# Optimization experiments

Hardware: AMD Instinct MI355X
Metric: run time of the kernel (lower is better)

Reference implementation:

```python
import jax, jax.numpy as jnp
import numpy as np

SIZE_DICT = 512
DIM_DICT = 64
TEMPERATURE = 0.5
EPS = 1e-10


def setup_inputs() -> dict:
    key = jax.random.key(0)
    k1, k2, k3 = jax.random.split(key, 3)
    bs, dz, W, H = 32, 64, 32, 32
    z = jax.random.normal(k1, (bs, dz, W, H), dtype=jnp.float32)
    var_q = jnp.ones((1,), dtype=jnp.float32)
    codebook = jax.random.normal(k2, (SIZE_DICT, DIM_DICT), dtype=jnp.float32)
    gumbel_u = jax.random.uniform(k3, (bs * W * H, SIZE_DICT), dtype=jnp.float32)
    return {"z_from_encoder": z, "var_q": var_q, "codebook": codebook, "gumbel_u": gumbel_u}


def reference(z_from_encoder, var_q, codebook, gumbel_u):
    bs, dz, W, H = z_from_encoder.shape
    # permute to channels-last and flatten: [N, D]
    z_flat = jnp.transpose(z_from_encoder, (0, 2, 3, 1)).reshape(-1, dz)
    # precision with clamping as in torch code
    precision_q = jnp.clip(1.0 / jnp.clip(var_q, 1e-5, None), None, 1e5)  # [1]
    half_prec = 0.5 * precision_q
    # squared euclidean distances to codebook: [N, K]
    dist = (jnp.sum(z_flat ** 2, axis=1, keepdims=True)
            + jnp.sum(codebook ** 2, axis=1)
            - 2.0 * z_flat @ codebook.T)
    logit = -half_prec * dist
    logit = logit - jnp.max(logit, axis=-1, keepdims=True)
    logit = jnp.clip(logit, -50.0, 50.0)
    probabilities = jax.nn.softmax(logit, axis=-1)
    log_probabilities = jax.nn.log_softmax(logit, axis=-1)
    # Gumbel-softmax sampling (training path)
    g = -jnp.log(-jnp.log(gumbel_u + EPS) + EPS)
    encodings = jax.nn.softmax((logit + g) / TEMPERATURE, axis=-1)
    # soft codebook lookup
    z_quantized = (encodings @ codebook).reshape(bs, W, H, dz)
    z_to_decoder = jnp.transpose(z_quantized, (0, 3, 1, 2))  # [bs, D, W, H]
    # discrete KLD term: sum_{n,k} p log p / bs
    kld_discrete = jnp.sum(probabilities * log_probabilities) / bs
    # continuous KLD term: mean over batch of weighted squared error
    kld_continuous = jnp.mean(
        jnp.sum((z_from_encoder - z_to_decoder) ** 2 * half_prec, axis=(1, 2, 3)))
    loss = kld_discrete + kld_continuous
    # perplexity from detached probabilities
    avg_probs = jnp.clip(jnp.mean(jax.lax.stop_gradient(probabilities), axis=0), 1e-10, None)
    perplexity = jnp.exp(-jnp.sum(avg_probs * jnp.log(avg_probs + 1e-10)))
    return z_to_decoder, loss, perplexity
```

## Files before the change

kernel.cpp:

```cpp
#include <hip/hip_runtime.h>


typedef _Float16 half8 __attribute__((ext_vector_type(8)));
typedef float f32x4 __attribute__((ext_vector_type(4)));

#define WS_B1   4096
#define WS_B2   20480
#define WS_PROB 36864
#define WS_LOSS 299008
#define WS_RED  303104
#define WS_NEED 319488

#define SMEM_PRE 24064
#define SMEM_FB  155136

#define LOG2E 1.4426950408889634f
#define LN2   0.6931471805599453f
#define C2G   1.4426950408889634e-10f

__device__ __forceinline__ float half_prec(const float* var_q) {
  float vq = var_q[0];
  float pq = fminf(1.0f / fmaxf(vq, 1e-5f), 1e5f);
  return 0.5f * pq;
}

__global__ void k_pre(const float* __restrict__ var_q,
                      const float* __restrict__ cb,
                      float* __restrict__ ws, int pre) {
  int t = threadIdx.x, wg = blockIdx.x;
  if (wg == 0) {
    float hp = half_prec(var_q);
    if (t == 0) ws[512] = 0.0f;
    ws[516 + t] = 0.0f;
    const float4* row = (const float4*)(cb + t * 64);
    float s = 0.0f;
    #pragma unroll
    for (int i = 0; i < 16; ++i) {
      float4 v = row[i];
      s += v.x*v.x + v.y*v.y + v.z*v.z + v.w*v.w;
    }
    ws[t] = hp * s * LOG2E;
  }
  if (!pre) return;
  int gid = wg * 512 + t;
  if (gid < 4096) {
    int l = gid & 63, grp = gid >> 6;
    int tt = grp >> 1, kk = grp & 1;
    int cc = l & 15, gg = l >> 4;
    const float* src = cb + (cc*32 + tt)*64 + kk*32 + gg*8;
    float4 v0 = *(const float4*)src;
    float4 v1 = *(const float4*)(src + 4);
    half8 h = { (_Float16)v0.x, (_Float16)v0.y, (_Float16)v0.z, (_Float16)v0.w,
                (_Float16)v1.x, (_Float16)v1.y, (_Float16)v1.z, (_Float16)v1.w };
    ((half8*)(ws + WS_B1))[gid] = h;
  } else {
    int F = gid - 4096;
    int l = F & 63, grp = F >> 6;
    int kt = grp >> 2, nt = grp & 3;
    int cc = l & 15, gg = l >> 4;
    int dim = nt*16 + cc;
    half8 h;
    #pragma unroll
    for (int j = 0; j < 8; ++j) {
      int kap = gg*8 + j;
      int code = ((kap & 15) << 5) + 2*kt + (kap >> 4);
      h[j] = (_Float16)cb[code*64 + dim];
    }
    ((half8*)(ws + WS_B2))[F] = h;
  }
}

template <int PRE>
__global__ __launch_bounds__(512) void k_main_t(
    const float* __restrict__ z, const float* __restrict__ vq,
    const float* __restrict__ cb, const float* __restrict__ gu,
    float* __restrict__ out, float* __restrict__ ws)
{
  extern __shared__ char smem[];
  constexpr int CB = PRE ? 0 : 131072;
  char*  chunkAll = smem + CB;
  float* pr   = (float*)(smem + CB + 20480);
  float* redM = (float*)(smem + CB + 22528);
  float* redS = (float*)(smem + CB + 23040);
  float* redP = (float*)(smem + CB + 23552);

  const int tid  = threadIdx.x;
  const int lane = tid & 63;
  const int wv   = tid >> 6;
  const int h    = wv & 1;
  const int p    = wv >> 1;
  const int c    = lane & 15;
  const int g    = lane >> 4;

  pr[tid] = 0.0f;

  const half8* B1;
  const half8* B2;
  if constexpr (PRE) {
    B1 = (const half8*)(ws + WS_B1);
    B2 = (const half8*)(ws + WS_B2);
  } else {
    _Float16* lB1 = (_Float16*)smem;
    _Float16* lB2 = (_Float16*)(smem + 65536);
    #pragma unroll
    for (int i = 0; i < 8; ++i) {
      int F = tid + 512*i;
      int l = F & 63, grp = F >> 6;
      int t = grp >> 1, kk = grp & 1;
      int cc = l & 15, gg = l >> 4;
      const float* src = cb + (cc*32 + t)*64 + kk*32 + gg*8;
      float4 v0 = *(const float4*)src;
      float4 v1 = *(const float4*)(src + 4);
      half8 hh = { (_Float16)v0.x, (_Float16)v0.y, (_Float16)v0.z, (_Float16)v0.w,
                   (_Float16)v1.x, (_Float16)v1.y, (_Float16)v1.z, (_Float16)v1.w };
      ((half8*)lB1)[F] = hh;
    }
    #pragma unroll
    for (int i = 0; i < 8; ++i) {
      int F = tid + 512*i;
      int l = F & 63, grp = F >> 6;
      int kt = grp >> 2, nt = grp & 3;
      int cc = l & 15, gg = l >> 4;
      int dim = nt*16 + cc;
      half8 hh;
      #pragma unroll
      for (int j = 0; j < 8; ++j) {
        int kap = gg*8 + j;
        int code = ((kap & 15) << 5) + 2*kt + (kap >> 4);
        hh[j] = (_Float16)cb[code*64 + dim];
      }
      ((half8*)lB2)[F] = hh;
    }
    B1 = (const half8*)lB1;
    B2 = (const half8*)lB2;
  }

  const float hp   = half_prec(vq);
  const float s2hp = 2.0f * hp * LOG2E;

  const int row0 = (blockIdx.x * 4 + p) * 16;
  const int b    = row0 >> 10;
  const int wh0  = row0 & 1023;

  _Float16* zc = (_Float16*)(chunkAll + p * 5120);

  float zr[8];
  {
    const float* zp = z + ((size_t)(b*64 + lane) << 10) + wh0 + 8*h;
    float4 v0 = *(const float4*)zp;
    float4 v1 = *(const float4*)(zp + 4);
    zr[0]=v0.x; zr[1]=v0.y; zr[2]=v0.z; zr[3]=v0.w;
    zr[4]=v1.x; zr[5]=v1.y; zr[6]=v1.z; zr[7]=v1.w;
  }
  #pragma unroll
  for (int s = 0; s < 8; ++s) zc[(8*h + s)*72 + lane] = (_Float16)(zr[s] * s2hp);

  __syncthreads();

  f32x4 acc[16];
  {
    const float4* hn = (const float4*)(ws + c*32 + h*16);
    #pragma unroll
    for (int u = 0; u < 4; ++u) {
      float4 h4 = hn[u];
      acc[4*u+0] = (f32x4){-h4.x, -h4.x, -h4.x, -h4.x};
      acc[4*u+1] = (f32x4){-h4.y, -h4.y, -h4.y, -h4.y};
      acc[4*u+2] = (f32x4){-h4.z, -h4.z, -h4.z, -h4.z};
      acc[4*u+3] = (f32x4){-h4.w, -h4.w, -h4.w, -h4.w};
    }
  }

  half8 zA0 = *(const half8*)(zc + c*72 + g*8);
  half8 zA1 = *(const half8*)(zc + c*72 + 32 + g*8);

  #pragma unroll
  for (int t = 0; t < 16; ++t) {
    int tt = h*16 + t;
    acc[t] = __builtin_amdgcn_mfma_f32_16x16x32_f16(zA0, B1[(tt*2+0)*64 + lane], acc[t], 0, 0, 0);
    acc[t] = __builtin_amdgcn_mfma_f32_16x16x32_f16(zA1, B1[(tt*2+1)*64 + lane], acc[t], 0, 0, 0);
  }

  const float* gub = gu + ((size_t)(row0 + 4*g))*512 + c*32 + h*16;
  float4 ubA[4], ubB[4];
  #pragma unroll
  for (int tt = 0; tt < 4; ++tt) ubA[tt] = *(const float4*)(gub + tt*4);

  const int rix = p*32 + h*16;

  #pragma unroll
  for (int q = 0; q < 4; ++q) {
    float m = acc[0][q];
    #pragma unroll
    for (int t = 1; t < 16; ++t) m = fmaxf(m, acc[t][q]);
    #pragma unroll
    for (int o = 8; o > 0; o >>= 1) m = fmaxf(m, __shfl_xor(m, o));
    if (c == 0) redM[rix + 4*g + q] = m;
  }
  __syncthreads();
  float mq[4];
  #pragma unroll
  for (int q = 0; q < 4; ++q)
    mq[q] = fmaxf(redM[p*32 + 4*g + q], redM[p*32 + 16 + 4*g + q]);

  {
    float s1[4] = {0,0,0,0}, pl[4] = {0,0,0,0};
    #pragma unroll
    for (int t = 0; t < 16; ++t)
      #pragma unroll
      for (int q = 0; q < 4; ++q) {
        float l = acc[t][q] - mq[q];
        float e = exp2f(l);
        s1[q] += e;
        pl[q] = fmaf(e, l, pl[q]);
        acc[t][q] = e;
      }
    #pragma unroll
    for (int q = 0; q < 4; ++q) {
      #pragma unroll
      for (int o = 8; o > 0; o >>= 1) { s1[q] += __shfl_xor(s1[q], o); pl[q] += __shfl_xor(pl[q], o); }
      if (c == 0) { redS[rix + 4*g + q] = s1[q]; redP[rix + 4*g + q] = pl[q]; }
    }
  }
  __syncthreads();
  float kd = 0.0f, inv1[4];
  #pragma unroll
  for (int q = 0; q < 4; ++q) {
    float S = redS[p*32 + 4*g + q] + redS[p*32 + 16 + 4*g + q];
    float P = redP[p*32 + 4*g + q] + redP[p*32 + 16 + 4*g + q];
    inv1[q] = 1.0f / S;
    kd += P * inv1[q] - __log2f(S);
  }

  #pragma unroll
  for (int t = 0; t < 16; ++t) {
    float v = 0.0f;
    #pragma unroll
    for (int q = 0; q < 4; ++q) v = fmaf(acc[t][q], inv1[q], v);
    v += __shfl_xor(v, 16);
    v += __shfl_xor(v, 32);
    if (g == 0) atomicAdd(&pr[(h*16 + t)*16 + c], v);
  }

  #pragma unroll
  for (int q = 0; q < 4; ++q) {
    const float4* cur = (q & 1) ? ubB : ubA;
    float4*       nxt = (q & 1) ? ubA : ubB;
    if (q < 3) {
      #pragma unroll
      for (int tt = 0; tt < 4; ++tt) nxt[tt] = *(const float4*)(gub + (q+1)*512 + tt*4);
    }
    #pragma unroll
    for (int tt = 0; tt < 4; ++tt) {
      float4 u4 = cur[tt];
      float y0 = C2G - __log2f(u4.x + 1e-10f);
      float y1 = C2G - __log2f(u4.y + 1e-10f);
      float y2 = C2G - __log2f(u4.z + 1e-10f);
      float y3 = C2G - __log2f(u4.w + 1e-10f);
      float t0 = acc[4*tt+0][q] * __builtin_amdgcn_rcpf(y0);
      float t1 = acc[4*tt+1][q] * __builtin_amdgcn_rcpf(y1);
      float t2 = acc[4*tt+2][q] * __builtin_amdgcn_rcpf(y2);
      float t3 = acc[4*tt+3][q] * __builtin_amdgcn_rcpf(y3);
      acc[4*tt+0][q] = t0*t0;
      acc[4*tt+1][q] = t1*t1;
      acc[4*tt+2][q] = t2*t2;
      acc[4*tt+3][q] = t3*t3;
    }
  }

  __syncthreads();

  #pragma unroll
  for (int q = 0; q < 4; ++q) {
    float s = 0.0f;
    #pragma unroll
    for (int t = 0; t < 16; ++t) s += acc[t][q];
    #pragma unroll
    for (int o = 8; o > 0; o >>= 1) s += __shfl_xor(s, o);
    if (c == 0) redS[rix + 4*g + q] = s;
  }
  __syncthreads();
  #pragma unroll
  for (int q = 0; q < 4; ++q) {
    float inv = 1.0f / (redS[p*32 + 4*g + q] + redS[p*32 + 16 + 4*g + q]);
    #pragma unroll
    for (int t = 0; t < 16; ++t) acc[t][q] *= inv;
  }

  f32x4 zacc[4];
  #pragma unroll
  for (int nt = 0; nt < 4; ++nt) zacc[nt] = (f32x4){0.f, 0.f, 0.f, 0.f};

  _Float16* myES = (_Float16*)(chunkAll + wv * 2560);
  #pragma unroll
  for (int k = 0; k < 8; ++k) {
    _Float16* eS = myES + (k & 1) * 640;
    #pragma unroll
    for (int tb = 0; tb < 2; ++tb)
      #pragma unroll
      for (int q = 0; q < 4; ++q)
        eS[(4*g + q)*40 + 16*tb + c] = (_Float16)acc[2*k + tb][q];
    half8 ea = *(const half8*)(eS + c*40 + g*8);
    int kt = h*8 + k;
    #pragma unroll
    for (int nt = 0; nt < 4; ++nt)
      zacc[nt] = __builtin_amdgcn_mfma_f32_16x16x32_f16(ea, B2[(kt*4 + nt)*64 + lane], zacc[nt], 0, 0, 0);
  }

  __syncthreads();
  float* zqx = (float*)chunkAll + p * 1056;
  if (h) {
    #pragma unroll
    for (int nt = 0; nt < 4; ++nt)
      #pragma unroll
      for (int q = 0; q < 4; ++q)
        zqx[(4*g + q)*66 + nt*16 + c] = zacc[nt][q];
  }
  __syncthreads();
  if (!h) {
    #pragma unroll
    for (int nt = 0; nt < 4; ++nt)
      #pragma unroll
      for (int q = 0; q < 4; ++q) {
        int ix = (4*g + q)*66 + nt*16 + c;
        zqx[ix] += zacc[nt][q];
      }
  }
  __syncthreads();

  float kc = 0.0f;
  {
    float* orow = out + ((size_t)(b*64 + lane) << 10) + wh0 + 8*h;
    float4 o0, o1;
    o0.x = zqx[(8*h + 0)*66 + lane]; o0.y = zqx[(8*h + 1)*66 + lane];
    o0.z = zqx[(8*h + 2)*66 + lane]; o0.w = zqx[(8*h + 3)*66 + lane];
    o1.x = zqx[(8*h + 4)*66 + lane]; o1.y = zqx[(8*h + 5)*66 + lane];
    o1.z = zqx[(8*h + 6)*66 + lane]; o1.w = zqx[(8*h + 7)*66 + lane];
    float d;
    d = zr[0]-o0.x; kc = fmaf(d,d,kc);  d = zr[1]-o0.y; kc = fmaf(d,d,kc);
    d = zr[2]-o0.z; kc = fmaf(d,d,kc);  d = zr[3]-o0.w; kc = fmaf(d,d,kc);
    d = zr[4]-o1.x; kc = fmaf(d,d,kc);  d = zr[5]-o1.y; kc = fmaf(d,d,kc);
    d = zr[6]-o1.z; kc = fmaf(d,d,kc);  d = zr[7]-o1.w; kc = fmaf(d,d,kc);
    *(float4*)orow       = o0;
    *(float4*)(orow + 4) = o1;
  }
  kc *= hp;

  float lv = (h ? 0.0f : kd * (0.0625f * LN2)) + kc;
  #pragma unroll
  for (int o = 32; o > 0; o >>= 1) lv += __shfl_xor(lv, o);
  if (lane == 0) {
    if constexpr (PRE) ws[WS_LOSS + blockIdx.x*8 + wv] = lv;
    else               atomicAdd(&ws[512], lv);
  }

  __syncthreads();
  if constexpr (PRE) {
    ws[WS_PROB + (size_t)blockIdx.x*512 + tid] = pr[tid];
  } else {
    atomicAdd(ws + 516 + tid, pr[tid]);
  }
}

__global__ void k_red(float* __restrict__ ws) {
  int gix = blockIdx.x, t = threadIdx.x;
  float s = 0.0f;
  #pragma unroll 4
  for (int i = 0; i < 16; ++i) s += ws[WS_PROB + (size_t)(gix*16 + i)*512 + t];
  ws[WS_RED + gix*512 + t] = s;
}

__global__ void k_fin(const float* __restrict__ ws, float* __restrict__ out, int pre) {
  __shared__ float redH[16], redL[16];
  int t = threadIdx.x;
  float h = 0.0f, l = 0.0f;
  if (pre) {
    if (t < 512) {
      float s = 0.0f;
      #pragma unroll
      for (int g = 0; g < 32; ++g) s += ws[WS_RED + g*512 + t];
      float a = fmaxf(s * (1.0f/32768.0f), 1e-10f);
      h = -a * __logf(a + 1e-10f);
    } else {
      int x = t - 512;
      #pragma unroll
      for (int i = 0; i < 8; ++i) l += ws[WS_LOSS + x + 512*i];
    }
  } else {
    if (t < 512) {
      float a = fmaxf(ws[516 + t] * (1.0f/32768.0f), 1e-10f);
      h = -a * __logf(a + 1e-10f);
    } else if (t == 512) {
      l = ws[512];
    }
  }
  #pragma unroll
  for (int o = 32; o > 0; o >>= 1) { h += __shfl_xor(h, o); l += __shfl_xor(l, o); }
  if ((t & 63) == 0) { redH[t >> 6] = h; redL[t >> 6] = l; }
  __syncthreads();
  if (t == 0) {
    float H = 0.0f, L = 0.0f;
    #pragma unroll
    for (int i = 0; i < 16; ++i) { H += redH[i]; L += redL[i]; }
    out[2097152] = L * (1.0f/32.0f);
    out[2097153] = __expf(H);
  }
}

extern "C" void kernel_launch(void* const* d_in, const int* in_sizes, int n_in,
                              void* d_out, int out_size, void* d_ws, size_t ws_size,
                              hipStream_t stream) {
  const float* z  = (const float*)d_in[0];
  const float* vq = (const float*)d_in[1];
  const float* cb = (const float*)d_in[2];
  const float* gu = (const float*)d_in[3];
  float* out = (float*)d_out;
  float* ws  = (float*)d_ws;
  int pre = (ws_size >= (size_t)WS_NEED * 4) ? 1 : 0;

  hipLaunchKernelGGL(k_pre, dim3(16), dim3(512), 0, stream, vq, cb, ws, pre);
  if (pre) {
    hipLaunchKernelGGL(k_main_t<1>, dim3(512), dim3(512), SMEM_PRE, stream, z, vq, cb, gu, out, ws);
    hipLaunchKernelGGL(k_red, dim3(32), dim3(512), 0, stream, ws);
  } else {
    hipFuncSetAttribute((const void*)&k_main_t<0>, hipFuncAttributeMaxDynamicSharedMemorySize, SMEM_FB);
    hipLaunchKernelGGL(k_main_t<0>, dim3(512), dim3(512), SMEM_FB, stream, z, vq, cb, gu, out, ws);
  }
  hipLaunchKernelGGL(k_fin, dim3(1), dim3(1024), 0, stream, ws, out, pre);
}
```

Before: 65.42 us.

## Split each row chunk across four waves with 1024-thread blocks

The precomputed-codebook path now uses 1024-thread blocks, so four waves share each 16-row chunk instead of two. Each wave handles 128 codes, which halves the accumulator registers per wave and raises the wave count. Cross-wave max, sum and z-quantized reductions are extended to four partials, with an extra shared-memory staging buffer. The gumbel prefetch double-buffering is dropped in favour of direct loads. The fallback path is split out into its own non-templated kernel.

```diff
diff --git a/kernel.cpp b/kernel.cpp
--- a/kernel.cpp
+++ b/kernel.cpp
@@ -11,7 +11,15 @@
 #define WS_RED  303104
 #define WS_NEED 319488
 
-#define SMEM_PRE 24064
+#define ZC_OFF  0
+#define ES_OFF  9216
+#define ZQ_OFF  50176
+#define PR_OFF  83968
+#define RM_OFF  86016
+#define RS_OFF  87040
+#define RP_OFF  88064
+#define LB_OFF  89088
+#define SMEM_PRE 89152
 #define SMEM_FB  155136
 
 #define LOG2E 1.4426950408889634f
@@ -70,70 +78,30 @@
   }
 }
 
-template <int PRE>
-__global__ __launch_bounds__(512) void k_main_t(
+__global__ __launch_bounds__(1024) void k_main_pre(
     const float* __restrict__ z, const float* __restrict__ vq,
     const float* __restrict__ cb, const float* __restrict__ gu,
     float* __restrict__ out, float* __restrict__ ws)
 {
   extern __shared__ char smem[];
-  constexpr int CB = PRE ? 0 : 131072;
-  char*  chunkAll = smem + CB;
-  float* pr   = (float*)(smem + CB + 20480);
-  float* redM = (float*)(smem + CB + 22528);
-  float* redS = (float*)(smem + CB + 23040);
-  float* redP = (float*)(smem + CB + 23552);
+  float* pr   = (float*)(smem + PR_OFF);
+  float* redM = (float*)(smem + RM_OFF);
+  float* redS = (float*)(smem + RS_OFF);
+  float* redP = (float*)(smem + RP_OFF);
+  float* lb   = (float*)(smem + LB_OFF);
 
   const int tid  = threadIdx.x;
   const int lane = tid & 63;
   const int wv   = tid >> 6;
-  const int h    = wv & 1;
-  const int p    = wv >> 1;
+  const int e    = wv & 3;
+  const int p    = wv >> 2;
   const int c    = lane & 15;
   const int g    = lane >> 4;
 
-  pr[tid] = 0.0f;
-
-  const half8* B1;
-  const half8* B2;
-  if constexpr (PRE) {
-    B1 = (const half8*)(ws + WS_B1);
-    B2 = (const half8*)(ws + WS_B2);
-  } else {
-    _Float16* lB1 = (_Float16*)smem;
-    _Float16* lB2 = (_Float16*)(smem + 65536);
-    #pragma unroll
-    for (int i = 0; i < 8; ++i) {
-      int F = tid + 512*i;
-      int l = F & 63, grp = F >> 6;
-      int t = grp >> 1, kk = grp & 1;
-      int cc = l & 15, gg = l >> 4;
-      const float* src = cb + (cc*32 + t)*64 + kk*32 + gg*8;
-      float4 v0 = *(const float4*)src;
-      float4 v1 = *(const float4*)(src + 4);
-      half8 hh = { (_Float16)v0.x, (_Float16)v0.y, (_Float16)v0.z, (_Float16)v0.w,
-                   (_Float16)v1.x, (_Float16)v1.y, (_Float16)v1.z, (_Float16)v1.w };
-      ((half8*)lB1)[F] = hh;
-    }
-    #pragma unroll
-    for (int i = 0; i < 8; ++i) {
-      int F = tid + 512*i;
-      int l = F & 63, grp = F >> 6;
-      int kt = grp >> 2, nt = grp & 3;
-      int cc = l & 15, gg = l >> 4;
-      int dim = nt*16 + cc;
-      half8 hh;
-      #pragma unroll
-      for (int j = 0; j < 8; ++j) {
-        int kap = gg*8 + j;
-        int code = ((kap & 15) << 5) + 2*kt + (kap >> 4);
-        hh[j] = (_Float16)cb[code*64 + dim];
-      }
-      ((half8*)lB2)[F] = hh;
-    }
-    B1 = (const half8*)lB1;
-    B2 = (const half8*)lB2;
-  }
+  if (tid < 512) pr[tid] = 0.0f;
+
+  const half8* B1 = (const half8*)(ws + WS_B1);
+  const half8* B2 = (const half8*)(ws + WS_B2);
 
   const float hp   = half_prec(vq);
   const float s2hp = 2.0f * hp * LOG2E;
@@ -142,26 +110,24 @@
   const int b    = row0 >> 10;
   const int wh0  = row0 & 1023;
 
-  _Float16* zc = (_Float16*)(chunkAll + p * 5120);
-
-  float zr[8];
-  {
-    const float* zp = z + ((size_t)(b*64 + lane) << 10) + wh0 + 8*h;
+  _Float16* zc = (_Float16*)(smem + ZC_OFF + p * 2304);
+
+  float zr[4];
+  {
+    const float* zp = z + ((size_t)(b*64 + lane) << 10) + wh0 + 4*e;
     float4 v0 = *(const float4*)zp;
-    float4 v1 = *(const float4*)(zp + 4);
     zr[0]=v0.x; zr[1]=v0.y; zr[2]=v0.z; zr[3]=v0.w;
-    zr[4]=v1.x; zr[5]=v1.y; zr[6]=v1.z; zr[7]=v1.w;
-  }
-  #pragma unroll
-  for (int s = 0; s < 8; ++s) zc[(8*h + s)*72 + lane] = (_Float16)(zr[s] * s2hp);
-
-  __syncthreads();
-
-  f32x4 acc[16];
-  {
-    const float4* hn = (const float4*)(ws + c*32 + h*16);
-    #pragma unroll
-    for (int u = 0; u < 4; ++u) {
+  }
+  #pragma unroll
+  for (int s = 0; s < 4; ++s) zc[(4*e + s)*72 + lane] = (_Float16)(zr[s] * s2hp);
+
+  __syncthreads();
+
+  f32x4 acc[8];
+  {
+    const float4* hn = (const float4*)(ws + c*32 + 8*e);
+    #pragma unroll
+    for (int u = 0; u < 2; ++u) {
       float4 h4 = hn[u];
       acc[4*u+0] = (f32x4){-h4.x, -h4.x, -h4.x, -h4.x};
       acc[4*u+1] = (f32x4){-h4.y, -h4.y, -h4.y, -h4.y};
@@ -174,24 +140,19 @@
   half8 zA1 = *(const half8*)(zc + c*72 + 32 + g*8);
 
   #pragma unroll
-  for (int t = 0; t < 16; ++t) {
-    int tt = h*16 + t;
+  for (int t = 0; t < 8; ++t) {
+    int tt = 8*e + t;
     acc[t] = __builtin_amdgcn_mfma_f32_16x16x32_f16(zA0, B1[(tt*2+0)*64 + lane], acc[t], 0, 0, 0);
     acc[t] = __builtin_amdgcn_mfma_f32_16x16x32_f16(zA1, B1[(tt*2+1)*64 + lane], acc[t], 0, 0, 0);
   }
 
-  const float* gub = gu + ((size_t)(row0 + 4*g))*512 + c*32 + h*16;
-  float4 ubA[4], ubB[4];
-  #pragma unroll
-  for (int tt = 0; tt < 4; ++tt) ubA[tt] = *(const float4*)(gub + tt*4);
-
-  const int rix = p*32 + h*16;
+  const int rix = p*64 + e*16;
 
   #pragma unroll
   for (int q = 0; q < 4; ++q) {
     float m = acc[0][q];
     #pragma unroll
-    for (int t = 1; t < 16; ++t) m = fmaxf(m, acc[t][q]);
+    for (int t = 1; t < 8; ++t) m = fmaxf(m, acc[t][q]);
     #pragma unroll
     for (int o = 8; o > 0; o >>= 1) m = fmaxf(m, __shfl_xor(m, o));
     if (c == 0) redM[rix + 4*g + q] = m;
@@ -199,20 +160,22 @@
   __syncthreads();
   float mq[4];
   #pragma unroll
-  for (int q = 0; q < 4; ++q)
-    mq[q] = fmaxf(redM[p*32 + 4*g + q], redM[p*32 + 16 + 4*g + q]);
+  for (int q = 0; q < 4; ++q) {
+    int ix = p*64 + 4*g + q;
+    mq[q] = fmaxf(fmaxf(redM[ix], redM[ix+16]), fmaxf(redM[ix+32], redM[ix+48]));
+  }
 
   {
     float s1[4] = {0,0,0,0}, pl[4] = {0,0,0,0};
     #pragma unroll
-    for (int t = 0; t < 16; ++t)
+    for (int t = 0; t < 8; ++t)
       #pragma unroll
       for (int q = 0; q < 4; ++q) {
         float l = acc[t][q] - mq[q];
-        float e = exp2f(l);
-        s1[q] += e;
-        pl[q] = fmaf(e, l, pl[q]);
-        acc[t][q] = e;
+        float ev = exp2f(l);
+        s1[q] += ev;
+        pl[q] = fmaf(ev, l, pl[q]);
+        acc[t][q] = ev;
       }
     #pragma unroll
     for (int q = 0; q < 4; ++q) {
@@ -225,33 +188,29 @@
   float kd = 0.0f, inv1[4];
   #pragma unroll
   for (int q = 0; q < 4; ++q) {
-    float S = redS[p*32 + 4*g + q] + redS[p*32 + 16 + 4*g + q];
-    float P = redP[p*32 + 4*g + q] + redP[p*32 + 16 + 4*g + q];
+    int ix = p*64 + 4*g + q;
+    float S = (redS[ix] + redS[ix+16]) + (redS[ix+32] + redS[ix+48]);
+    float P = (redP[ix] + redP[ix+16]) + (redP[ix+32] + redP[ix+48]);
     inv1[q] = 1.0f / S;
     kd += P * inv1[q] - __log2f(S);
   }
 
   #pragma unroll
-  for (int t = 0; t < 16; ++t) {
+  for (int t = 0; t < 8; ++t) {
     float v = 0.0f;
     #pragma unroll
     for (int q = 0; q < 4; ++q) v = fmaf(acc[t][q], inv1[q], v);
     v += __shfl_xor(v, 16);
     v += __shfl_xor(v, 32);
-    if (g == 0) atomicAdd(&pr[(h*16 + t)*16 + c], v);
-  }
-
-  #pragma unroll
-  for (int q = 0; q < 4; ++q) {
-    const float4* cur = (q & 1) ? ubB : ubA;
-    float4*       nxt = (q & 1) ? ubA : ubB;
-    if (q < 3) {
-      #pragma unroll
-      for (int tt = 0; tt < 4; ++tt) nxt[tt] = *(const float4*)(gub + (q+1)*512 + tt*4);
-    }
-    #pragma unroll
-    for (int tt = 0; tt < 4; ++tt) {
-      float4 u4 = cur[tt];
+    if (g == 0) atomicAdd(&pr[(8*e + t)*16 + c], v);
+  }
+
+  #pragma unroll
+  for (int q = 0; q < 4; ++q) {
+    const float4* ub = (const float4*)(gu + ((size_t)(row0 + 4*g + q))*512 + c*32 + 8*e);
+    #pragma unroll
+    for (int tt = 0; tt < 2; ++tt) {
+      float4 u4 = ub[tt];
       float y0 = C2G - __log2f(u4.x + 1e-10f);
       float y1 = C2G - __log2f(u4.y + 1e-10f);
       float y2 = C2G - __log2f(u4.z + 1e-10f);
@@ -273,6 +232,272 @@
   for (int q = 0; q < 4; ++q) {
     float s = 0.0f;
     #pragma unroll
+    for (int t = 0; t < 8; ++t) s += acc[t][q];
+    #pragma unroll
+    for (int o = 8; o > 0; o >>= 1) s += __shfl_xor(s, o);
+    if (c == 0) redS[rix + 4*g + q] = s;
+  }
+  __syncthreads();
+  #pragma unroll
+  for (int q = 0; q < 4; ++q) {
+    int ix = p*64 + 4*g + q;
+    float inv = 1.0f / ((redS[ix] + redS[ix+16]) + (redS[ix+32] + redS[ix+48]));
+    #pragma unroll
+    for (int t = 0; t < 8; ++t) acc[t][q] *= inv;
+  }
+
+  f32x4 zacc[4];
+  #pragma unroll
+  for (int nt = 0; nt < 4; ++nt) zacc[nt] = (f32x4){0.f, 0.f, 0.f, 0.f};
+
+  _Float16* myES = (_Float16*)(smem + ES_OFF + wv * 2560);
+  #pragma unroll
+  for (int k = 0; k < 4; ++k) {
+    _Float16* eS = myES + (k & 1) * 640;
+    #pragma unroll
+    for (int tb = 0; tb < 2; ++tb)
+      #pragma unroll
+      for (int q = 0; q < 4; ++q)
+        eS[(4*g + q)*40 + 16*tb + c] = (_Float16)acc[2*k + tb][q];
+    half8 ea = *(const half8*)(eS + c*40 + g*8);
+    int kt = 4*e + k;
+    #pragma unroll
+    for (int nt = 0; nt < 4; ++nt)
+      zacc[nt] = __builtin_amdgcn_mfma_f32_16x16x32_f16(ea, B2[(kt*4 + nt)*64 + lane], zacc[nt], 0, 0, 0);
+  }
+
+  float* zqA = (float*)(smem + ZQ_OFF + p * 8448);
+  float* zqB = zqA + 1056;
+  if (e & 1) {
+    float* zqX = (e == 1) ? zqA : zqB;
+    #pragma unroll
+    for (int nt = 0; nt < 4; ++nt)
+      #pragma unroll
+      for (int q = 0; q < 4; ++q)
+        zqX[(4*g + q)*66 + nt*16 + c] = zacc[nt][q];
+  }
+  __syncthreads();
+  if (!(e & 1)) {
+    float* zqX = (e == 0) ? zqA : zqB;
+    #pragma unroll
+    for (int nt = 0; nt < 4; ++nt)
+      #pragma unroll
+      for (int q = 0; q < 4; ++q)
+        zqX[(4*g + q)*66 + nt*16 + c] += zacc[nt][q];
+  }
+  __syncthreads();
+
+  float kc = 0.0f;
+  {
+    float* orow = out + ((size_t)(b*64 + lane) << 10) + wh0 + 4*e;
+    float4 ov;
+    ov.x = zqA[(4*e + 0)*66 + lane] + zqB[(4*e + 0)*66 + lane];
+    ov.y = zqA[(4*e + 1)*66 + lane] + zqB[(4*e + 1)*66 + lane];
+    ov.z = zqA[(4*e + 2)*66 + lane] + zqB[(4*e + 2)*66 + lane];
+    ov.w = zqA[(4*e + 3)*66 + lane] + zqB[(4*e + 3)*66 + lane];
+    float d;
+    d = zr[0]-ov.x; kc = fmaf(d,d,kc);  d = zr[1]-ov.y; kc = fmaf(d,d,kc);
+    d = zr[2]-ov.z; kc = fmaf(d,d,kc);  d = zr[3]-ov.w; kc = fmaf(d,d,kc);
+    *(float4*)orow = ov;
+  }
+  kc *= hp;
+
+  float lv = ((e == 0) ? kd * (0.0625f * LN2) : 0.0f) + kc;
+  #pragma unroll
+  for (int o = 32; o > 0; o >>= 1) lv += __shfl_xor(lv, o);
+  if (lane == 0) lb[p*4 + e] = lv;
+  __syncthreads();
+  if (e == 0 && lane == 0)
+    ws[WS_LOSS + blockIdx.x*4 + p] = (lb[p*4+0] + lb[p*4+1]) + (lb[p*4+2] + lb[p*4+3]);
+
+  if (tid < 512) ws[WS_PROB + (size_t)blockIdx.x*512 + tid] = pr[tid];
+}
+
+__global__ __launch_bounds__(512) void k_main_fb(
+    const float* __restrict__ z, const float* __restrict__ vq,
+    const float* __restrict__ cb, const float* __restrict__ gu,
+    float* __restrict__ out, float* __restrict__ ws)
+{
+  extern __shared__ char smem[];
+  constexpr int CB = 131072;
+  char*  chunkAll = smem + CB;
+  float* pr   = (float*)(smem + CB + 20480);
+  float* redM = (float*)(smem + CB + 22528);
+  float* redS = (float*)(smem + CB + 23040);
+  float* redP = (float*)(smem + CB + 23552);
+
+  const int tid  = threadIdx.x;
+  const int lane = tid & 63;
+  const int wv   = tid >> 6;
+  const int h    = wv & 1;
+  const int p    = wv >> 1;
+  const int c    = lane & 15;
+  const int g    = lane >> 4;
+
+  pr[tid] = 0.0f;
+
+  _Float16* lB1 = (_Float16*)smem;
+  _Float16* lB2 = (_Float16*)(smem + 65536);
+  #pragma unroll
+  for (int i = 0; i < 8; ++i) {
+    int F = tid + 512*i;
+    int l = F & 63, grp = F >> 6;
+    int t = grp >> 1, kk = grp & 1;
+    int cc = l & 15, gg = l >> 4;
+    const float* src = cb + (cc*32 + t)*64 + kk*32 + gg*8;
+    float4 v0 = *(const float4*)src;
+    float4 v1 = *(const float4*)(src + 4);
+    half8 hh = { (_Float16)v0.x, (_Float16)v0.y, (_Float16)v0.z, (_Float16)v0.w,
+                 (_Float16)v1.x, (_Float16)v1.y, (_Float16)v1.z, (_Float16)v1.w };
+    ((half8*)lB1)[F] = hh;
+  }
+  #pragma unroll
+  for (int i = 0; i < 8; ++i) {
+    int F = tid + 512*i;
+    int l = F & 63, grp = F >> 6;
+    int kt = grp >> 2, nt = grp & 3;
+    int cc = l & 15, gg = l >> 4;
+    int dim = nt*16 + cc;
+    half8 hh;
+    #pragma unroll
+    for (int j = 0; j < 8; ++j) {
+      int kap = gg*8 + j;
+      int code = ((kap & 15) << 5) + 2*kt + (kap >> 4);
+      hh[j] = (_Float16)cb[code*64 + dim];
+    }
+    ((half8*)lB2)[F] = hh;
+  }
+  const half8* B1 = (const half8*)lB1;
+  const half8* B2 = (const half8*)lB2;
+
+  const float hp   = half_prec(vq);
+  const float s2hp = 2.0f * hp * LOG2E;
+
+  const int row0 = (blockIdx.x * 4 + p) * 16;
+  const int b    = row0 >> 10;
+  const int wh0  = row0 & 1023;
+
+  _Float16* zc = (_Float16*)(chunkAll + p * 5120);
+
+  float zr[8];
+  {
+    const float* zp = z + ((size_t)(b*64 + lane) << 10) + wh0 + 8*h;
+    float4 v0 = *(const float4*)zp;
+    float4 v1 = *(const float4*)(zp + 4);
+    zr[0]=v0.x; zr[1]=v0.y; zr[2]=v0.z; zr[3]=v0.w;
+    zr[4]=v1.x; zr[5]=v1.y; zr[6]=v1.z; zr[7]=v1.w;
+  }
+  #pragma unroll
+  for (int s = 0; s < 8; ++s) zc[(8*h + s)*72 + lane] = (_Float16)(zr[s] * s2hp);
+
+  __syncthreads();
+
+  f32x4 acc[16];
+  {
+    const float4* hn = (const float4*)(ws + c*32 + h*16);
+    #pragma unroll
+    for (int u = 0; u < 4; ++u) {
+      float4 h4 = hn[u];
+      acc[4*u+0] = (f32x4){-h4.x, -h4.x, -h4.x, -h4.x};
+      acc[4*u+1] = (f32x4){-h4.y, -h4.y, -h4.y, -h4.y};
+      acc[4*u+2] = (f32x4){-h4.z, -h4.z, -h4.z, -h4.z};
+      acc[4*u+3] = (f32x4){-h4.w, -h4.w, -h4.w, -h4.w};
+    }
+  }
+
+  half8 zA0 = *(const half8*)(zc + c*72 + g*8);
+  half8 zA1 = *(const half8*)(zc + c*72 + 32 + g*8);
+
+  #pragma unroll
+  for (int t = 0; t < 16; ++t) {
+    int tt = h*16 + t;
+    acc[t] = __builtin_amdgcn_mfma_f32_16x16x32_f16(zA0, B1[(tt*2+0)*64 + lane], acc[t], 0, 0, 0);
+    acc[t] = __builtin_amdgcn_mfma_f32_16x16x32_f16(zA1, B1[(tt*2+1)*64 + lane], acc[t], 0, 0, 0);
+  }
+
+  const int rix = p*32 + h*16;
+
+  #pragma unroll
+  for (int q = 0; q < 4; ++q) {
+    float m = acc[0][q];
+    #pragma unroll
+    for (int t = 1; t < 16; ++t) m = fmaxf(m, acc[t][q]);
+    #pragma unroll
+    for (int o = 8; o > 0; o >>= 1) m = fmaxf(m, __shfl_xor(m, o));
+    if (c == 0) redM[rix + 4*g + q] = m;
+  }
+  __syncthreads();
+  float mq[4];
+  #pragma unroll
+  for (int q = 0; q < 4; ++q)
+    mq[q] = fmaxf(redM[p*32 + 4*g + q], redM[p*32 + 16 + 4*g + q]);
+
+  {
+    float s1[4] = {0,0,0,0}, pl[4] = {0,0,0,0};
+    #pragma unroll
+    for (int t = 0; t < 16; ++t)
+      #pragma unroll
+      for (int q = 0; q < 4; ++q) {
+        float l = acc[t][q] - mq[q];
+        float ev = exp2f(l);
+        s1[q] += ev;
+        pl[q] = fmaf(ev, l, pl[q]);
+        acc[t][q] = ev;
+      }
+    #pragma unroll
+    for (int q = 0; q < 4; ++q) {
+      #pragma unroll
+      for (int o = 8; o > 0; o >>= 1) { s1[q] += __shfl_xor(s1[q], o); pl[q] += __shfl_xor(pl[q], o); }
+      if (c == 0) { redS[rix + 4*g + q] = s1[q]; redP[rix + 4*g + q] = pl[q]; }
+    }
+  }
+  __syncthreads();
+  float kd = 0.0f, inv1[4];
+  #pragma unroll
+  for (int q = 0; q < 4; ++q) {
+    float S = redS[p*32 + 4*g + q] + redS[p*32 + 16 + 4*g + q];
+    float P = redP[p*32 + 4*g + q] + redP[p*32 + 16 + 4*g + q];
+    inv1[q] = 1.0f / S;
+    kd += P * inv1[q] - __log2f(S);
+  }
+
+  #pragma unroll
+  for (int t = 0; t < 16; ++t) {
+    float v = 0.0f;
+    #pragma unroll
+    for (int q = 0; q < 4; ++q) v = fmaf(acc[t][q], inv1[q], v);
+    v += __shfl_xor(v, 16);
+    v += __shfl_xor(v, 32);
+    if (g == 0) atomicAdd(&pr[(h*16 + t)*16 + c], v);
+  }
+
+  #pragma unroll
+  for (int q = 0; q < 4; ++q) {
+    const float4* ub = (const float4*)(gu + ((size_t)(row0 + 4*g + q))*512 + c*32 + h*16);
+    #pragma unroll
+    for (int tt = 0; tt < 4; ++tt) {
+      float4 u4 = ub[tt];
+      float y0 = C2G - __log2f(u4.x + 1e-10f);
+      float y1 = C2G - __log2f(u4.y + 1e-10f);
+      float y2 = C2G - __log2f(u4.z + 1e-10f);
+      float y3 = C2G - __log2f(u4.w + 1e-10f);
+      float t0 = acc[4*tt+0][q] * __builtin_amdgcn_rcpf(y0);
+      float t1 = acc[4*tt+1][q] * __builtin_amdgcn_rcpf(y1);
+      float t2 = acc[4*tt+2][q] * __builtin_amdgcn_rcpf(y2);
+      float t3 = acc[4*tt+3][q] * __builtin_amdgcn_rcpf(y3);
+      acc[4*tt+0][q] = t0*t0;
+      acc[4*tt+1][q] = t1*t1;
+      acc[4*tt+2][q] = t2*t2;
+      acc[4*tt+3][q] = t3*t3;
+    }
+  }
+
+  __syncthreads();
+
+  #pragma unroll
+  for (int q = 0; q < 4; ++q) {
+    float s = 0.0f;
+    #pragma unroll
     for (int t = 0; t < 16; ++t) s += acc[t][q];
     #pragma unroll
     for (int o = 8; o > 0; o >>= 1) s += __shfl_xor(s, o);
@@ -320,10 +545,8 @@
     #pragma unroll
     for (int nt = 0; nt < 4; ++nt)
       #pragma unroll
-      for (int q = 0; q < 4; ++q) {
-        int ix = (4*g + q)*66 + nt*16 + c;
-        zqx[ix] += zacc[nt][q];
-      }
+      for (int q = 0; q < 4; ++q)
+        zqx[(4*g + q)*66 + nt*16 + c] += zacc[nt][q];
   }
   __syncthreads();
 
@@ -348,17 +571,10 @@
   float lv = (h ? 0.0f : kd * (0.0625f * LN2)) + kc;
   #pragma unroll
   for (int o = 32; o > 0; o >>= 1) lv += __shfl_xor(lv, o);
-  if (lane == 0) {
-    if constexpr (PRE) ws[WS_LOSS + blockIdx.x*8 + wv] = lv;
-    else               atomicAdd(&ws[512], lv);
-  }
-
-  __syncthreads();
-  if constexpr (PRE) {
-    ws[WS_PROB + (size_t)blockIdx.x*512 + tid] = pr[tid];
-  } else {
-    atomicAdd(ws + 516 + tid, pr[tid]);
-  }
+  if (lane == 0) atomicAdd(&ws[512], lv);
+
+  __syncthreads();
+  atomicAdd(ws + 516 + tid, pr[tid]);
 }
 
 __global__ void k_red(float* __restrict__ ws) {
@@ -383,7 +599,7 @@
     } else {
       int x = t - 512;
       #pragma unroll
-      for (int i = 0; i < 8; ++i) l += ws[WS_LOSS + x + 512*i];
+      for (int i = 0; i < 4; ++i) l += ws[WS_LOSS + x + 512*i];
     }
   } else {
     if (t < 512) {
@@ -419,11 +635,12 @@
 
   hipLaunchKernelGGL(k_pre, dim3(16), dim3(512), 0, stream, vq, cb, ws, pre);
   if (pre) {
-    hipLaunchKernelGGL(k_main_t<1>, dim3(512), dim3(512), SMEM_PRE, stream, z, vq, cb, gu, out, ws);
+    hipFuncSetAttribute((const void*)k_main_pre, hipFuncAttributeMaxDynamicSharedMemorySize, SMEM_PRE);
+    hipLaunchKernelGGL(k_main_pre, dim3(512), dim3(1024), SMEM_PRE, stream, z, vq, cb, gu, out, ws);
     hipLaunchKernelGGL(k_red, dim3(32), dim3(512), 0, stream, ws);
   } else {
-    hipFuncSetAttribute((const void*)&k_main_t<0>, hipFuncAttributeMaxDynamicSharedMemorySize, SMEM_FB);
-    hipLaunchKernelGGL(k_main_t<0>, dim3(512), dim3(512), SMEM_FB, stream, z, vq, cb, gu, out, ws);
+    hipFuncSetAttribute((const void*)k_main_fb, hipFuncAttributeMaxDynamicSharedMemorySize, SMEM_FB);
+    hipLaunchKernelGGL(k_main_fb, dim3(512), dim3(512), SMEM_FB, stream, z, vq, cb, gu, out, ws);
   }
   hipLaunchKernelGGL(k_fin, dim3(1), dim3(1024), 0, stream, ws, out, pre);
 }
```

Result: faster. 62.52 us (-4.4%).

## Stage gumbel noise tile into LDS with async global_load_lds and swizzle

Applied to the files above, without the earlier changes.

In the precomputed path, the whole 64x512 gumbel-uniform tile for a block is copied into LDS with asynchronous global-to-LDS loads, issued before the MFMA distance computation. The Gumbel stage then reads it from LDS through an XOR swizzle that avoids bank conflicts. This replaces the register double-buffered global loads and hides their latency behind the matmul. In exchange every block now reserves about 155KB of LDS instead of about 24KB, which likely caps occupancy at one block per CU.

```diff
diff --git a/kernel.cpp b/kernel.cpp
--- a/kernel.cpp
+++ b/kernel.cpp
@@ -1,4 +1,5 @@
 #include <hip/hip_runtime.h>
+#include <stdint.h>
 
 
 typedef _Float16 half8 __attribute__((ext_vector_type(8)));
@@ -11,8 +12,12 @@
 #define WS_RED  303104
 #define WS_NEED 319488
 
-#define SMEM_PRE 24064
-#define SMEM_FB  155136
+#define CH_OFF  131072
+#define PR_OFF  151552
+#define RM_OFF  153600
+#define RS_OFF  154112
+#define RP_OFF  154624
+#define SMEM_ALL 155136
 
 #define LOG2E 1.4426950408889634f
 #define LN2   0.6931471805599453f
@@ -22,6 +27,12 @@
   float vq = var_q[0];
   float pq = fminf(1.0f / fmaxf(vq, 1e-5f), 1e5f);
   return 0.5f * pq;
+}
+
+__device__ __forceinline__ void async16(void* l, const void* g) {
+  __builtin_amdgcn_global_load_lds(
+      (const __attribute__((address_space(1))) uint32_t*)g,
+      (__attribute__((address_space(3))) uint32_t*)l, 16, 0, 0);
 }
 
 __global__ void k_pre(const float* __restrict__ var_q,
@@ -77,12 +88,11 @@
     float* __restrict__ out, float* __restrict__ ws)
 {
   extern __shared__ char smem[];
-  constexpr int CB = PRE ? 0 : 131072;
-  char*  chunkAll = smem + CB;
-  float* pr   = (float*)(smem + CB + 20480);
-  float* redM = (float*)(smem + CB + 22528);
-  float* redS = (float*)(smem + CB + 23040);
-  float* redP = (float*)(smem + CB + 23552);
+  char*  chunkAll = smem + CH_OFF;
+  float* pr   = (float*)(smem + PR_OFF);
+  float* redM = (float*)(smem + RM_OFF);
+  float* redS = (float*)(smem + RS_OFF);
+  float* redP = (float*)(smem + RP_OFF);
 
   const int tid  = threadIdx.x;
   const int lane = tid & 63;
@@ -157,6 +167,16 @@
 
   __syncthreads();
 
+  if constexpr (PRE) {
+    const char* gub = (const char*)(gu + (size_t)blockIdx.x * 64 * 512);
+    #pragma unroll
+    for (int i = 0; i < 16; ++i) {
+      int L  = i*512 + tid;
+      int Gs = L ^ ((L >> 3) & 7);
+      async16(smem + (size_t)L*16, gub + (size_t)Gs*16);
+    }
+  }
+
   f32x4 acc[16];
   {
     const float4* hn = (const float4*)(ws + c*32 + h*16);
@@ -179,11 +199,6 @@
     acc[t] = __builtin_amdgcn_mfma_f32_16x16x32_f16(zA0, B1[(tt*2+0)*64 + lane], acc[t], 0, 0, 0);
     acc[t] = __builtin_amdgcn_mfma_f32_16x16x32_f16(zA1, B1[(tt*2+1)*64 + lane], acc[t], 0, 0, 0);
   }
-
-  const float* gub = gu + ((size_t)(row0 + 4*g))*512 + c*32 + h*16;
-  float4 ubA[4], ubB[4];
-  #pragma unroll
-  for (int tt = 0; tt < 4; ++tt) ubA[tt] = *(const float4*)(gub + tt*4);
 
   const int rix = p*32 + h*16;
 
@@ -243,15 +258,21 @@
 
   #pragma unroll
   for (int q = 0; q < 4; ++q) {
-    const float4* cur = (q & 1) ? ubB : ubA;
-    float4*       nxt = (q & 1) ? ubA : ubB;
-    if (q < 3) {
-      #pragma unroll
-      for (int tt = 0; tt < 4; ++tt) nxt[tt] = *(const float4*)(gub + (q+1)*512 + tt*4);
+    float4 u4s[4];
+    if constexpr (PRE) {
+      const float4* guL = (const float4*)smem;
+      int Sb = (p*16 + 4*g + q)*128 + c*8 + h*4;
+      int sx = c & 7;
+      #pragma unroll
+      for (int tt = 0; tt < 4; ++tt) u4s[tt] = guL[(Sb + tt) ^ sx];
+    } else {
+      const float4* ub = (const float4*)(gu + ((size_t)(row0 + 4*g + q))*512 + c*32 + h*16);
+      #pragma unroll
+      for (int tt = 0; tt < 4; ++tt) u4s[tt] = ub[tt];
     }
     #pragma unroll
     for (int tt = 0; tt < 4; ++tt) {
-      float4 u4 = cur[tt];
+      float4 u4 = u4s[tt];
       float y0 = C2G - __log2f(u4.x + 1e-10f);
       float y1 = C2G - __log2f(u4.y + 1e-10f);
       float y2 = C2G - __log2f(u4.z + 1e-10f);
@@ -419,11 +440,12 @@
 
   hipLaunchKernelGGL(k_pre, dim3(16), dim3(512), 0, stream, vq, cb, ws, pre);
   if (pre) {
-    hipLaunchKernelGGL(k_main_t<1>, dim3(512), dim3(512), SMEM_PRE, stream, z, vq, cb, gu, out, ws);
+    hipFuncSetAttribute((const void*)&k_main_t<1>, hipFuncAttributeMaxDynamicSharedMemorySize, SMEM_ALL);
+    hipLaunchKernelGGL(k_main_t<1>, dim3(512), dim3(512), SMEM_ALL, stream, z, vq, cb, gu, out, ws);
     hipLaunchKernelGGL(k_red, dim3(32), dim3(512), 0, stream, ws);
   } else {
-    hipFuncSetAttribute((const void*)&k_main_t<0>, hipFuncAttributeMaxDynamicSharedMemorySize, SMEM_FB);
-    hipLaunchKernelGGL(k_main_t<0>, dim3(512), dim3(512), SMEM_FB, stream, z, vq, cb, gu, out, ws);
+    hipFuncSetAttribute((const void*)&k_main_t<0>, hipFuncAttributeMaxDynamicSharedMemorySize, SMEM_ALL);
+    hipLaunchKernelGGL(k_main_t<0>, dim3(512), dim3(512), SMEM_ALL, stream, z, vq, cb, gu, out, ws);
   }
   hipLaunchKernelGGL(k_fin, dim3(1), dim3(1024), 0, stream, ws, out, pre);
 }
```

Result: faster. 60.73 us (-7.2%).
